# Optimization experiments

Hardware: AMD Instinct MI355X
Metric: run time of the kernel (lower is better)

The kernel has to match this reference:

```python
import jax, jax.numpy as jnp
import numpy as np

DIM = 1024
HEADS = 16
DIM_HEAD = 64
INNER = HEADS * DIM_HEAD
SCALE = DIM_HEAD ** -0.5


def setup_inputs() -> dict:
    key = jax.random.key(0)
    ks = jax.random.split(key, 7)
    B, S = 2, 2048
    x = jax.random.normal(ks[0], (B, S, DIM), dtype=jnp.float32)
    mask = jax.random.bernoulli(ks[1], 0.9, (B, S, S))  # bool [B,Q,K]
    init = lambda k, shape: jax.random.normal(k, shape, dtype=jnp.float32) * (shape[0] ** -0.5)
    Wq = init(ks[2], (DIM, INNER))
    Wk = init(ks[3], (DIM, INNER))
    Wv = init(ks[4], (DIM, INNER))
    Wo = init(ks[5], (INNER, DIM))
    bo = jnp.zeros((DIM,), dtype=jnp.float32)
    return {"x": x, "mask": mask, "Wq": Wq, "Wk": Wk, "Wv": Wv, "Wo": Wo, "bo": bo}


def reference(x, mask, Wq, Wk, Wv, Wo, bo):
    B, S, _ = x.shape
    # projections -> [B, H, S, Dh]
    q = (x @ Wq).reshape(B, S, HEADS, DIM_HEAD).transpose(0, 2, 1, 3)
    k = (x @ Wk).reshape(B, S, HEADS, DIM_HEAD).transpose(0, 2, 1, 3)
    v = (x @ Wv).reshape(B, S, HEADS, DIM_HEAD).transpose(0, 2, 1, 3)
    sim = jnp.einsum('bhid,bhjd->bhij', q, k) * SCALE
    attn_mask = mask[:, None]  # [B,1,Q,K]
    neg = -jnp.finfo(sim.dtype).max
    sim = jnp.where(attn_mask, sim, neg)
    attn = jax.nn.softmax(sim, axis=-1)
    # post-hoc mask renormalization
    attn = attn * attn_mask.astype(attn.dtype)
    attn = attn / jnp.maximum(attn.sum(axis=-1, keepdims=True), 1e-9)
    out = jnp.einsum('bhij,bhjd->bhid', attn, v)
    out = out.transpose(0, 2, 1, 3).reshape(B, S, INNER)
    return out @ Wo + bo
```

## Files before the change

kernel.cpp:

```cpp
#include <hip/hip_runtime.h>
#include <stdint.h>

#define SEQ 2048
#define DM 1024
#define NHEAD 16
#define HD 64

typedef __attribute__((ext_vector_type(8))) __bf16 bf16x8;
typedef __attribute__((ext_vector_type(4))) __bf16 bf16x4;
typedef __attribute__((ext_vector_type(4))) float f32x4;
typedef __attribute__((ext_vector_type(4))) short s16x4;
typedef __attribute__((ext_vector_type(4))) unsigned short u16x4;
typedef __attribute__((ext_vector_type(8))) unsigned short u16x8;
typedef __attribute__((ext_vector_type(4))) unsigned int u32x4;
typedef __attribute__((ext_vector_type(2))) unsigned int u32x2;

__device__ __forceinline__ unsigned short f2b(float f) {
  unsigned u = __builtin_bit_cast(unsigned, f);
  return (unsigned short)((u + 0x7FFFu + ((u >> 16) & 1u)) >> 16);
}

__device__ __forceinline__ float exp2_raw(float x) {
#if __has_builtin(__builtin_amdgcn_exp2f)
  return __builtin_amdgcn_exp2f(x);
#else
  float r;
  asm("v_exp_f32 %0, %1" : "=v"(r) : "v"(x));
  return r;
#endif
}

__device__ __forceinline__ void gload16(const void* g, void* l) {
  __builtin_amdgcn_global_load_lds((__attribute__((address_space(1))) void*)g,
                                   (__attribute__((address_space(3))) void*)l,
                                   16, 0, 0);
}


__global__ __launch_bounds__(256) void k_conv_x(const float* __restrict__ x,
                                                unsigned short* __restrict__ xb) {
  size_t i = (size_t)blockIdx.x * 256 + threadIdx.x;
  const f32x4* xv = (const f32x4*)x;
  f32x4 a = xv[i * 2], b = xv[i * 2 + 1];
  u16x8 o;
  o[0] = f2b(a[0]); o[1] = f2b(a[1]); o[2] = f2b(a[2]); o[3] = f2b(a[3]);
  o[4] = f2b(b[0]); o[5] = f2b(b[1]); o[6] = f2b(b[2]); o[7] = f2b(b[3]);
  ((u16x8*)xb)[i] = o;
}

__global__ __launch_bounds__(256) void k_conv_wt(const float* __restrict__ W0,
                                                 const float* __restrict__ W1,
                                                 const float* __restrict__ W2,
                                                 const float* __restrict__ W3,
                                                 unsigned short* __restrict__ out) {
  __shared__ float t[32][33];
  int z = blockIdx.z;
  const float* W = (z == 0) ? W0 : (z == 1) ? W1 : (z == 2) ? W2 : W3;
  unsigned short* o = out + (size_t)z * DM * DM;
  int tid = threadIdx.x;
  int r = tid >> 3, c4 = (tid & 7) << 2;
  f32x4 v = *(const f32x4*)&W[(size_t)(blockIdx.y * 32 + r) * DM + blockIdx.x * 32 + c4];
  t[r][c4 + 0] = v[0]; t[r][c4 + 1] = v[1]; t[r][c4 + 2] = v[2]; t[r][c4 + 3] = v[3];
  __syncthreads();
  u16x4 ov;
  ov[0] = f2b(t[c4 + 0][r]); ov[1] = f2b(t[c4 + 1][r]);
  ov[2] = f2b(t[c4 + 2][r]); ov[3] = f2b(t[c4 + 3][r]);
  *(u16x4*)&o[(size_t)(blockIdx.x * 32 + r) * DM + blockIdx.y * 32 + c4] = ov;
}

__global__ __launch_bounds__(256) void k_maskpack(const void* __restrict__ maskp,
                                                  unsigned* __restrict__ bits) {
  const int lane = threadIdx.x & 63;
  const int wv = blockIdx.x * 4 + (threadIdx.x >> 6);
  const unsigned* pw = (const unsigned*)maskp;
  unsigned s = pw[(size_t)wv * 512 + lane];
  unsigned long long ba = __ballot(s <= 1u);
  unsigned long long bf = __ballot(s == 0x3f800000u);
  bool dword = (bf != 0ull) || (ba == ~0ull);
  if (dword) {
    for (int gi = 0; gi < 32; ++gi) {
      unsigned d = pw[(size_t)wv * 2048 + gi * 64 + lane];
      unsigned long long bal = __ballot(d != 0u);
      if (lane == 0) bits[wv * 64 + gi * 2] = (unsigned)bal;
      if (lane == 32) bits[wv * 64 + gi * 2 + 1] = (unsigned)(bal >> 32);
    }
  } else {
    int wid = wv * 64 + lane;
    const u32x4* p = (const u32x4*)((const uint8_t*)maskp + (size_t)wid * 32);
    u32x4 v0 = p[0], v1 = p[1];
    unsigned word = 0;
    #pragma unroll
    for (int e = 0; e < 4; ++e) {
      unsigned d = v0[e];
      #pragma unroll
      for (int by = 0; by < 4; ++by)
        word |= (((d >> (8 * by)) & 0xffu) ? 1u : 0u) << (4 * e + by);
      d = v1[e];
      #pragma unroll
      for (int by = 0; by < 4; ++by)
        word |= (((d >> (8 * by)) & 0xffu) ? 1u : 0u) << (16 + 4 * e + by);
    }
    bits[wid] = word;
  }
}


#define BM 128
#define BN 128
#define BK 64

__device__ __forceinline__ void stage_tile64(const unsigned short* __restrict__ src,
                                             int row0, int kk, void* lds, int tid) {
  #pragma unroll
  for (int i = 0; i < 4; ++i) {
    int row = i * 32 + (tid >> 3);
    int cs = (tid & 7) ^ (row & 7);
    gload16(src + (size_t)(row0 + row) * DM + kk + cs * 8, (char*)lds + i * 4096 + tid * 16);
  }
}

__global__ __launch_bounds__(256) void k_gemm_qkv(const unsigned short* __restrict__ A,
                                                  const unsigned short* __restrict__ Wt,
                                                  unsigned short* __restrict__ Qb,
                                                  unsigned short* __restrict__ Kb,
                                                  unsigned short* __restrict__ Vt) {
  __shared__ __align__(16) unsigned short As[BM * BK];
  __shared__ __align__(16) unsigned short Bs[BN * BK];
  int z = blockIdx.y;
  const unsigned short* Bt = Wt + (size_t)z * DM * DM;
  int tid = threadIdx.x;
  int lane = tid & 63, w = tid >> 6;
  int li = lane & 15, g = lane >> 4;
  int bm = blockIdx.x >> 3, bn = blockIdx.x & 7;
  int row0 = bm * BM, col0 = bn * BN;
  int m0 = (w >> 1) * 64, n0 = (w & 1) * 64;
  f32x4 acc[4][4];
  #pragma unroll
  for (int i = 0; i < 4; ++i)
    #pragma unroll
    for (int j = 0; j < 4; ++j) acc[i][j] = (f32x4){0.f, 0.f, 0.f, 0.f};

  for (int kk = 0; kk < DM; kk += BK) {
    stage_tile64(A, row0, kk, As, tid);
    stage_tile64(Bt, col0, kk, Bs, tid);
    __syncthreads();
    #pragma unroll
    for (int kk2 = 0; kk2 < 2; ++kk2) {
      bf16x8 af[4], bfr[4];
      #pragma unroll
      for (int mi = 0; mi < 4; ++mi)
        af[mi] = *(const bf16x8*)((const char*)As + (m0 + mi * 16 + li) * 128 +
                                  (((kk2 * 4 + g) ^ (li & 7)) << 4));
      #pragma unroll
      for (int ni = 0; ni < 4; ++ni)
        bfr[ni] = *(const bf16x8*)((const char*)Bs + (n0 + ni * 16 + li) * 128 +
                                   (((kk2 * 4 + g) ^ (li & 7)) << 4));
      #pragma unroll
      for (int mi = 0; mi < 4; ++mi)
        #pragma unroll
        for (int ni = 0; ni < 4; ++ni)
          acc[mi][ni] = __builtin_amdgcn_mfma_f32_16x16x32_bf16(af[mi], bfr[ni], acc[mi][ni], 0, 0, 0);
    }
    __syncthreads();
  }

  if (z == 2) {
    #pragma unroll
    for (int mi = 0; mi < 4; ++mi)
      #pragma unroll
      for (int ni = 0; ni < 4; ++ni) {
        int mb = row0 + m0 + mi * 16 + g * 4;
        int n = col0 + n0 + ni * 16 + li;
        int bb = mb >> 11, s = mb & 2047;
        u16x4 ov;
        #pragma unroll
        for (int r = 0; r < 4; ++r) ov[r] = f2b(acc[mi][ni][r]);
        *(u16x4*)&Vt[((size_t)(bb * DM + n)) * SEQ + s] = ov;
      }
  } else {
    unsigned short* O = (z == 0) ? Qb : Kb;
    float sc = (z == 0) ? 0.18033688f : 1.0f;
    #pragma unroll
    for (int mi = 0; mi < 4; ++mi)
      #pragma unroll
      for (int ni = 0; ni < 4; ++ni) {
        int n = col0 + n0 + ni * 16 + li;
        #pragma unroll
        for (int r = 0; r < 4; ++r) {
          int m = row0 + m0 + mi * 16 + g * 4 + r;
          O[(size_t)m * DM + n] = f2b(acc[mi][ni][r] * sc);
        }
      }
  }
}

__global__ __launch_bounds__(256) void k_gemm_o(const unsigned short* __restrict__ A,
                                                const unsigned short* __restrict__ Bt,
                                                const float* __restrict__ bo,
                                                float* __restrict__ out) {
  __shared__ __align__(16) unsigned short As[BM * BK];
  __shared__ __align__(16) unsigned short Bs[BN * BK];
  int tid = threadIdx.x;
  int lane = tid & 63, w = tid >> 6;
  int li = lane & 15, g = lane >> 4;
  int bm = blockIdx.x >> 3, bn = blockIdx.x & 7;
  int row0 = bm * BM, col0 = bn * BN;
  int m0 = (w >> 1) * 64, n0 = (w & 1) * 64;
  f32x4 acc[4][4];
  #pragma unroll
  for (int i = 0; i < 4; ++i)
    #pragma unroll
    for (int j = 0; j < 4; ++j) acc[i][j] = (f32x4){0.f, 0.f, 0.f, 0.f};

  for (int kk = 0; kk < DM; kk += BK) {
    stage_tile64(A, row0, kk, As, tid);
    stage_tile64(Bt, col0, kk, Bs, tid);
    __syncthreads();
    #pragma unroll
    for (int kk2 = 0; kk2 < 2; ++kk2) {
      bf16x8 af[4], bfr[4];
      #pragma unroll
      for (int mi = 0; mi < 4; ++mi)
        af[mi] = *(const bf16x8*)((const char*)As + (m0 + mi * 16 + li) * 128 +
                                  (((kk2 * 4 + g) ^ (li & 7)) << 4));
      #pragma unroll
      for (int ni = 0; ni < 4; ++ni)
        bfr[ni] = *(const bf16x8*)((const char*)Bs + (n0 + ni * 16 + li) * 128 +
                                   (((kk2 * 4 + g) ^ (li & 7)) << 4));
      #pragma unroll
      for (int mi = 0; mi < 4; ++mi)
        #pragma unroll
        for (int ni = 0; ni < 4; ++ni)
          acc[mi][ni] = __builtin_amdgcn_mfma_f32_16x16x32_bf16(af[mi], bfr[ni], acc[mi][ni], 0, 0, 0);
    }
    __syncthreads();
  }

  #pragma unroll
  for (int mi = 0; mi < 4; ++mi)
    #pragma unroll
    for (int ni = 0; ni < 4; ++ni) {
      int n = col0 + n0 + ni * 16 + li;
      float bias = bo[n];
      #pragma unroll
      for (int r = 0; r < 4; ++r) {
        int m = row0 + m0 + mi * 16 + g * 4 + r;
        out[(size_t)m * DM + n] = acc[mi][ni][r] + bias;
      }
    }
}

__global__ __launch_bounds__(256) void k_attn(const unsigned short* __restrict__ Qm,
                                              const unsigned short* __restrict__ Km,
                                              const unsigned short* __restrict__ Vt,
                                              const unsigned* __restrict__ bits,
                                              unsigned short* __restrict__ AO) {
  __shared__ __align__(16) char kvbuf[2][16384];
  const int tid = threadIdx.x;
  const int lane = tid & 63;
  const int w = tid >> 6;
  const int li = lane & 15, g = lane >> 4;
  unsigned id = blockIdx.x;
  unsigned swz = (id & 7) * 64 + (id >> 3);
  const int qb = swz & 15;
  const int h = (swz >> 4) & 15;
  const int b = swz >> 8;
  const int q0 = qb * 128;
  const size_t qrow0w = (size_t)b * SEQ + q0 + w * 32;

  const char* Kg = (const char*)Km + ((size_t)b * SEQ * DM + h * HD) * 2;
  const char* Vg = (const char*)Vt + ((size_t)(b * DM + h * HD)) * SEQ * 2;

  auto stage = [&](int buf, int kb) {
    char* base = &kvbuf[buf][0];
    #pragma unroll
    for (int i = 0; i < 2; ++i) {
      int o = (w * 2 + i) * 1024 + lane * 16;
      int row = o >> 7, c = (o >> 4) & 7;
      int cs = (c ^ (row & 7)) << 4;
      gload16(Kg + (size_t)(kb + row) * 2048 + cs, base + o);
      gload16(Vg + (size_t)row * 4096 + (size_t)kb * 2 + cs, base + 8192 + o);
    }
  };

  bf16x8 qf[2][2];
  #pragma unroll
  for (int is = 0; is < 2; ++is)
    #pragma unroll
    for (int kc = 0; kc < 2; ++kc)
      qf[is][kc] = *(const bf16x8*)(Qm + (qrow0w + is * 16 + li) * DM + h * HD + kc * 32 + g * 8);

  f32x4 acc[2][4];
  f32x4 accl[2];
  #pragma unroll
  for (int is = 0; is < 2; ++is) {
    #pragma unroll
    for (int ds = 0; ds < 4; ++ds) acc[is][ds] = (f32x4){0.f, 0.f, 0.f, 0.f};
    accl[is] = (f32x4){0.f, 0.f, 0.f, 0.f};
  }
  bf16x4 onesb;
  onesb[0] = onesb[1] = onesb[2] = onesb[3] = (li == 0) ? (__bf16)1.0f : (__bf16)0.0f;
  const s16x4 ones = __builtin_bit_cast(s16x4, onesb);

  const unsigned* mr[2] = {bits + (qrow0w + li) * (SEQ / 32),
                           bits + (qrow0w + 16 + li) * (SEQ / 32)};
  const int sh0 = g * 4;

  stage(0, 0);
  __syncthreads();
  int cur = 0;

  for (int t = 0; t < SEQ / 64; ++t) {
    unsigned mw[2][2];
    #pragma unroll
    for (int is = 0; is < 2; ++is) {
      u32x2 mv = *(const u32x2*)(mr[is] + t * 2);
      mw[is][0] = mv[0];
      mw[is][1] = mv[1];
    }
    if (t + 1 < SEQ / 64) stage(cur ^ 1, (t + 1) * 64);

    const char* Kl = &kvbuf[cur][0];
    const char* Vl = &kvbuf[cur][8192];

    const f32x4 minit = (f32x4){-16.f, -16.f, -16.f, -16.f};
    f32x4 st[2][4];
    #pragma unroll
    for (int kt = 0; kt < 4; ++kt) {
      bf16x8 k0 = *(const bf16x8*)(Kl + (kt * 16 + li) * 128 + (((0 + g) ^ (li & 7)) << 4));
      bf16x8 k1 = *(const bf16x8*)(Kl + (kt * 16 + li) * 128 + (((4 + g) ^ (li & 7)) << 4));
      #pragma unroll
      for (int is = 0; is < 2; ++is) {
        st[is][kt] = __builtin_amdgcn_mfma_f32_16x16x32_bf16(k0, qf[is][0], minit, 0, 0, 0);
        st[is][kt] = __builtin_amdgcn_mfma_f32_16x16x32_bf16(k1, qf[is][1], st[is][kt], 0, 0, 0);
      }
    }

    s16x4 vf[4][4];
    #pragma unroll
    for (int ds = 0; ds < 4; ++ds)
      #pragma unroll
      for (int kt = 0; kt < 4; ++kt)
        vf[ds][kt] = *(const s16x4*)(Vl + (ds * 16 + li) * 128 +
                                     (((kt * 2 + (g >> 1)) ^ (li & 7)) << 4) + ((g & 1) << 3));

    #pragma unroll
    for (int is = 0; is < 2; ++is) {
      bf16x4 pb[4];
      #pragma unroll
      for (int kt = 0; kt < 4; ++kt) {
        unsigned mwv = mw[is][kt >> 1];
        #pragma unroll
        for (int r = 0; r < 4; ++r) {
          float ex = exp2_raw(st[is][kt][r]);
          int sext = __builtin_amdgcn_sbfe((int)mwv, (sh0 + (kt & 1) * 16 + r) & 31, 1);
          ex = __builtin_bit_cast(float, __builtin_bit_cast(int, ex) & sext);
          pb[kt][r] = (__bf16)ex;
        }
      }
      #pragma unroll
      for (int ds = 0; ds < 4; ++ds) {
        #pragma unroll
        for (int kt = 0; kt < 4; ++kt)
          acc[is][ds] = __builtin_amdgcn_mfma_f32_16x16x16bf16_1k(
              vf[ds][kt], __builtin_bit_cast(s16x4, pb[kt]), acc[is][ds], 0, 0, 0);
      }
      #pragma unroll
      for (int kt = 0; kt < 4; ++kt)
        accl[is] = __builtin_amdgcn_mfma_f32_16x16x16bf16_1k(
            ones, __builtin_bit_cast(s16x4, pb[kt]), accl[is], 0, 0, 0);
    }
    __syncthreads();
    cur ^= 1;
  }

  #pragma unroll
  for (int is = 0; is < 2; ++is) {
    float lv = __shfl(accl[is][0], li);
    float inv = 1.f / fmaxf(lv, 1e-9f);
    #pragma unroll
    for (int ds = 0; ds < 4; ++ds) {
      u16x4 ov;
      #pragma unroll
      for (int r = 0; r < 4; ++r) ov[r] = f2b(acc[is][ds][r] * inv);
      *(u16x4*)(AO + (qrow0w + is * 16 + li) * DM + h * HD + ds * 16 + g * 4) = ov;
    }
  }
}


extern "C" void kernel_launch(void* const* d_in, const int* in_sizes, int n_in,
                              void* d_out, int out_size, void* d_ws, size_t ws_size,
                              hipStream_t stream) {
  const float* x = (const float*)d_in[0];
  const void* mk = d_in[1];
  const float* Wq = (const float*)d_in[2];
  const float* Wk = (const float*)d_in[3];
  const float* Wv = (const float*)d_in[4];
  const float* Wo = (const float*)d_in[5];
  const float* bo = (const float*)d_in[6];
  float* out = (float*)d_out;
  char* ws = (char*)d_ws;

  unsigned short* xb = (unsigned short*)(ws);
  unsigned short* wt = (unsigned short*)(ws + ((size_t)8 << 20));
  unsigned short* Qb = (unsigned short*)(ws + ((size_t)16 << 20));
  unsigned short* Kb = (unsigned short*)(ws + ((size_t)24 << 20));
  unsigned short* Vt = (unsigned short*)(ws + ((size_t)32 << 20));
  unsigned* bits = (unsigned*)(ws + ((size_t)40 << 20));
  unsigned short* AO = xb;

  hipLaunchKernelGGL(k_conv_x, dim3(2048), dim3(256), 0, stream, x, xb);
  hipLaunchKernelGGL(k_conv_wt, dim3(32, 32, 4), dim3(256), 0, stream, Wq, Wk, Wv, Wo, wt);
  hipLaunchKernelGGL(k_maskpack, dim3(1024), dim3(256), 0, stream, mk, bits);
  hipLaunchKernelGGL(k_gemm_qkv, dim3(256, 3), dim3(256), 0, stream, xb, wt, Qb, Kb, Vt);
  hipLaunchKernelGGL(k_attn, dim3(512), dim3(256), 0, stream, Qb, Kb, Vt, bits, AO);
  hipLaunchKernelGGL(k_gemm_o, dim3(256), dim3(256), 0, stream, AO, wt + (size_t)3 * DM * DM, bo, out);
}
```

Measured before the change: 155.3 us.

## Merge prep kernels into one launch and swizzle GEMM block order

Combines the x conversion, weight transpose-conversion and mask packing into a single kernel that dispatches on block index, which removes two kernel launches and their gaps. The QKV and output GEMMs also remap block indices so that consecutive blocks walk along the M dimension within one N column, which is meant to improve L2 reuse of weight tiles. The fused kernel reserves shared memory for every block even though only the transpose blocks use it, which may slightly lower occupancy.

```diff
diff --git a/kernel.cpp b/kernel.cpp
--- a/kernel.cpp
+++ b/kernel.cpp
@@ -36,71 +36,73 @@
                                    16, 0, 0);
 }
 
-
-__global__ __launch_bounds__(256) void k_conv_x(const float* __restrict__ x,
-                                                unsigned short* __restrict__ xb) {
-  size_t i = (size_t)blockIdx.x * 256 + threadIdx.x;
-  const f32x4* xv = (const f32x4*)x;
-  f32x4 a = xv[i * 2], b = xv[i * 2 + 1];
-  u16x8 o;
-  o[0] = f2b(a[0]); o[1] = f2b(a[1]); o[2] = f2b(a[2]); o[3] = f2b(a[3]);
-  o[4] = f2b(b[0]); o[5] = f2b(b[1]); o[6] = f2b(b[2]); o[7] = f2b(b[3]);
-  ((u16x8*)xb)[i] = o;
-}
-
-__global__ __launch_bounds__(256) void k_conv_wt(const float* __restrict__ W0,
-                                                 const float* __restrict__ W1,
-                                                 const float* __restrict__ W2,
-                                                 const float* __restrict__ W3,
-                                                 unsigned short* __restrict__ out) {
+__global__ __launch_bounds__(256) void k_prep(const float* __restrict__ x,
+                                              const float* __restrict__ W0,
+                                              const float* __restrict__ W1,
+                                              const float* __restrict__ W2,
+                                              const float* __restrict__ W3,
+                                              const void* __restrict__ maskp,
+                                              unsigned short* __restrict__ xb,
+                                              unsigned short* __restrict__ wt,
+                                              unsigned* __restrict__ bits) {
   __shared__ float t[32][33];
-  int z = blockIdx.z;
-  const float* W = (z == 0) ? W0 : (z == 1) ? W1 : (z == 2) ? W2 : W3;
-  unsigned short* o = out + (size_t)z * DM * DM;
-  int tid = threadIdx.x;
-  int r = tid >> 3, c4 = (tid & 7) << 2;
-  f32x4 v = *(const f32x4*)&W[(size_t)(blockIdx.y * 32 + r) * DM + blockIdx.x * 32 + c4];
-  t[r][c4 + 0] = v[0]; t[r][c4 + 1] = v[1]; t[r][c4 + 2] = v[2]; t[r][c4 + 3] = v[3];
-  __syncthreads();
-  u16x4 ov;
-  ov[0] = f2b(t[c4 + 0][r]); ov[1] = f2b(t[c4 + 1][r]);
-  ov[2] = f2b(t[c4 + 2][r]); ov[3] = f2b(t[c4 + 3][r]);
-  *(u16x4*)&o[(size_t)(blockIdx.x * 32 + r) * DM + blockIdx.y * 32 + c4] = ov;
-}
-
-__global__ __launch_bounds__(256) void k_maskpack(const void* __restrict__ maskp,
-                                                  unsigned* __restrict__ bits) {
-  const int lane = threadIdx.x & 63;
-  const int wv = blockIdx.x * 4 + (threadIdx.x >> 6);
-  const unsigned* pw = (const unsigned*)maskp;
-  unsigned s = pw[(size_t)wv * 512 + lane];
-  unsigned long long ba = __ballot(s <= 1u);
-  unsigned long long bf = __ballot(s == 0x3f800000u);
-  bool dword = (bf != 0ull) || (ba == ~0ull);
-  if (dword) {
-    for (int gi = 0; gi < 32; ++gi) {
-      unsigned d = pw[(size_t)wv * 2048 + gi * 64 + lane];
-      unsigned long long bal = __ballot(d != 0u);
-      if (lane == 0) bits[wv * 64 + gi * 2] = (unsigned)bal;
-      if (lane == 32) bits[wv * 64 + gi * 2 + 1] = (unsigned)(bal >> 32);
-    }
+  const unsigned blk = blockIdx.x;
+  const int tid = threadIdx.x;
+
+  if (blk < 1024) {
+    const int lane = tid & 63;
+    const int wv = blk * 4 + (tid >> 6);
+    const unsigned* pw = (const unsigned*)maskp;
+    unsigned s = pw[(size_t)wv * 512 + lane];
+    unsigned long long ba = __ballot(s <= 1u);
+    unsigned long long bf = __ballot(s == 0x3f800000u);
+    bool dword = (bf != 0ull) || (ba == ~0ull);
+    if (dword) {
+      for (int gi = 0; gi < 32; ++gi) {
+        unsigned d = pw[(size_t)wv * 2048 + gi * 64 + lane];
+        unsigned long long bal = __ballot(d != 0u);
+        if (lane == 0) bits[wv * 64 + gi * 2] = (unsigned)bal;
+        if (lane == 32) bits[wv * 64 + gi * 2 + 1] = (unsigned)(bal >> 32);
+      }
+    } else {
+      int wid = wv * 64 + lane;
+      const u32x4* p = (const u32x4*)((const uint8_t*)maskp + (size_t)wid * 32);
+      u32x4 v0 = p[0], v1 = p[1];
+      unsigned word = 0;
+      #pragma unroll
+      for (int e = 0; e < 4; ++e) {
+        unsigned d = v0[e];
+        #pragma unroll
+        for (int by = 0; by < 4; ++by)
+          word |= (((d >> (8 * by)) & 0xffu) ? 1u : 0u) << (4 * e + by);
+        d = v1[e];
+        #pragma unroll
+        for (int by = 0; by < 4; ++by)
+          word |= (((d >> (8 * by)) & 0xffu) ? 1u : 0u) << (16 + 4 * e + by);
+      }
+      bits[wid] = word;
+    }
+  } else if (blk < 3072) {
+    size_t i = (size_t)(blk - 1024) * 256 + tid;
+    const f32x4* xv = (const f32x4*)x;
+    f32x4 a = xv[i * 2], b = xv[i * 2 + 1];
+    u16x8 o;
+    o[0] = f2b(a[0]); o[1] = f2b(a[1]); o[2] = f2b(a[2]); o[3] = f2b(a[3]);
+    o[4] = f2b(b[0]); o[5] = f2b(b[1]); o[6] = f2b(b[2]); o[7] = f2b(b[3]);
+    ((u16x8*)xb)[i] = o;
   } else {
-    int wid = wv * 64 + lane;
-    const u32x4* p = (const u32x4*)((const uint8_t*)maskp + (size_t)wid * 32);
-    u32x4 v0 = p[0], v1 = p[1];
-    unsigned word = 0;
-    #pragma unroll
-    for (int e = 0; e < 4; ++e) {
-      unsigned d = v0[e];
-      #pragma unroll
-      for (int by = 0; by < 4; ++by)
-        word |= (((d >> (8 * by)) & 0xffu) ? 1u : 0u) << (4 * e + by);
-      d = v1[e];
-      #pragma unroll
-      for (int by = 0; by < 4; ++by)
-        word |= (((d >> (8 * by)) & 0xffu) ? 1u : 0u) << (16 + 4 * e + by);
-    }
-    bits[wid] = word;
+    unsigned idx = blk - 3072;
+    int bx_ = idx & 31, by_ = (idx >> 5) & 31, z = idx >> 10;
+    const float* W = (z == 0) ? W0 : (z == 1) ? W1 : (z == 2) ? W2 : W3;
+    unsigned short* o = wt + (size_t)z * DM * DM;
+    int r = tid >> 3, c4 = (tid & 7) << 2;
+    f32x4 v = *(const f32x4*)&W[(size_t)(by_ * 32 + r) * DM + bx_ * 32 + c4];
+    t[r][c4 + 0] = v[0]; t[r][c4 + 1] = v[1]; t[r][c4 + 2] = v[2]; t[r][c4 + 3] = v[3];
+    __syncthreads();
+    u16x4 ov;
+    ov[0] = f2b(t[c4 + 0][r]); ov[1] = f2b(t[c4 + 1][r]);
+    ov[2] = f2b(t[c4 + 2][r]); ov[3] = f2b(t[c4 + 3][r]);
+    *(u16x4*)&o[(size_t)(bx_ * 32 + r) * DM + by_ * 32 + c4] = ov;
   }
 }
 
@@ -131,7 +133,9 @@
   int tid = threadIdx.x;
   int lane = tid & 63, w = tid >> 6;
   int li = lane & 15, g = lane >> 4;
-  int bm = blockIdx.x >> 3, bn = blockIdx.x & 7;
+  unsigned bx = blockIdx.x;
+  unsigned sw = (bx & 7) * 32 + (bx >> 3);
+  int bm = sw >> 3, bn = sw & 7;
   int row0 = bm * BM, col0 = bn * BN;
   int m0 = (w >> 1) * 64, n0 = (w & 1) * 64;
   f32x4 acc[4][4];
@@ -203,7 +207,9 @@
   int tid = threadIdx.x;
   int lane = tid & 63, w = tid >> 6;
   int li = lane & 15, g = lane >> 4;
-  int bm = blockIdx.x >> 3, bn = blockIdx.x & 7;
+  unsigned bx = blockIdx.x;
+  unsigned sw = (bx & 7) * 32 + (bx >> 3);
+  int bm = sw >> 3, bn = sw & 7;
   int row0 = bm * BM, col0 = bn * BN;
   int m0 = (w >> 1) * 64, n0 = (w & 1) * 64;
   f32x4 acc[4][4];
@@ -410,9 +416,8 @@
   unsigned* bits = (unsigned*)(ws + ((size_t)40 << 20));
   unsigned short* AO = xb;
 
-  hipLaunchKernelGGL(k_conv_x, dim3(2048), dim3(256), 0, stream, x, xb);
-  hipLaunchKernelGGL(k_conv_wt, dim3(32, 32, 4), dim3(256), 0, stream, Wq, Wk, Wv, Wo, wt);
-  hipLaunchKernelGGL(k_maskpack, dim3(1024), dim3(256), 0, stream, mk, bits);
+  hipLaunchKernelGGL(k_prep, dim3(7168), dim3(256), 0, stream,
+                     x, Wq, Wk, Wv, Wo, mk, xb, wt, bits);
   hipLaunchKernelGGL(k_gemm_qkv, dim3(256, 3), dim3(256), 0, stream, xb, wt, Qb, Kb, Vt);
   hipLaunchKernelGGL(k_attn, dim3(512), dim3(256), 0, stream, Qb, Kb, Vt, bits, AO);
   hipLaunchKernelGGL(k_gemm_o, dim3(256), dim3(256), 0, stream, AO, wt + (size_t)3 * DM * DM, bo, out);
```

After: 137.3 us. -11.6%, faster.
